# Kernel optimization log

Measured on AMD Instinct MI355X. Metric: run time of the kernel, lower is better.

Reference implementation:

```python
import jax, jax.numpy as jnp
import numpy as np

B, N, DIM = 2, 2048, 1024
HEADS, DIM_HEAD = 16, 64
ALIBI_HEADS = 8
NUM_MEM_KV = 4
SCALE = DIM_HEAD ** -0.5


def alibi_slopes(n):
    # standard ALiBi geometric slopes for power-of-2 head counts
    start = 2.0 ** (-8.0 / n)
    return jnp.array([start ** (k + 1) for k in range(n)], dtype=jnp.float32)


def alibi_bias(i, j, heads, total_heads):
    # symmetric ALiBi: bias = -|k_pos - q_pos| * slope; unbiased heads padded with zeros at front
    range_q = jnp.arange(j - i, j)          # query absolute positions (offset by mem kv)
    range_k = jnp.arange(j)
    rel = -jnp.abs(range_k[None, :] - range_q[:, None]).astype(jnp.float32)  # [i, j]
    slopes = alibi_slopes(heads)
    bias = slopes[:, None, None] * rel[None]                                  # [heads, i, j]
    pad = jnp.zeros((total_heads - heads, i, j), dtype=bias.dtype)
    return jnp.concatenate([pad, bias], axis=0)                               # [total_heads, i, j]


def setup_inputs() -> dict:
    key = jax.random.key(0)
    ks = jax.random.split(key, 7)
    w = lambda k, s: jax.random.normal(k, s, jnp.float32) * 0.02
    return {
        "x": jax.random.normal(ks[0], (B, N, DIM), jnp.float32),
        "mask": jnp.ones((B, N), dtype=bool),
        "Wq": w(ks[1], (DIM, HEADS * DIM_HEAD)),
        "Wk": w(ks[2], (DIM, HEADS * DIM_HEAD)),
        "Wv": w(ks[3], (DIM, HEADS * DIM_HEAD)),
        "Wo": w(ks[4], (HEADS * DIM_HEAD, DIM)),
        "mem_k": jax.random.normal(ks[5], (HEADS, NUM_MEM_KV, DIM_HEAD), jnp.float32),
        "mem_v": jax.random.normal(ks[6], (HEADS, NUM_MEM_KV, DIM_HEAD), jnp.float32),
    }


def reference(x, mask, Wq, Wk, Wv, Wo, mem_k, mem_v):
    b, n, _ = x.shape
    h, d, m = HEADS, DIM_HEAD, NUM_MEM_KV
    # QKV projections (Linear, no bias)
    q = (x @ Wq).reshape(b, n, h, d).transpose(0, 2, 1, 3)  # [b,h,n,d]
    k = (x @ Wk).reshape(b, n, h, d).transpose(0, 2, 1, 3)
    v = (x @ Wv).reshape(b, n, h, d).transpose(0, 2, 1, 3)
    # prepend learned memory key/values
    k = jnp.concatenate([jnp.broadcast_to(mem_k[None], (b, h, m, d)), k], axis=2)
    v = jnp.concatenate([jnp.broadcast_to(mem_v[None], (b, h, m, d)), v], axis=2)
    i, j = n, n + m
    # input mask padded with True over memory positions
    input_mask = jnp.concatenate([jnp.ones((b, m), dtype=bool), mask], axis=1)  # [b,j]
    # causal mask: key kj attendable by query qi iff kj - (j - i) <= qi (mem keys always visible)
    qpos = jnp.arange(i)[:, None]
    kpos = jnp.arange(j)[None, :]
    causal_allow = (kpos - (j - i)) <= qpos                                      # [i,j]
    allow = input_mask[:, None, None, :] & causal_allow[None, None]              # [b,1,i,j]
    bias = alibi_bias(i, j, ALIBI_HEADS, h)                                      # [h,i,j]
    scores = jnp.einsum('bhid,bhjd->bhij', q, k) * SCALE + bias[None]
    scores = jnp.where(allow, scores, jnp.finfo(scores.dtype).min)
    attn = jax.nn.softmax(scores, axis=-1)
    out = jnp.einsum('bhij,bhjd->bhid', attn, v)
    out = out.transpose(0, 2, 1, 3).reshape(b, n, h * d) @ Wo
    return out * mask[..., None].astype(out.dtype)
```

## Files before the change

kernel.cpp:

```cpp
#include <hip/hip_runtime.h>

typedef __bf16 bf16x8 __attribute__((ext_vector_type(8)));
typedef float f32x4 __attribute__((ext_vector_type(4)));
typedef unsigned short us8 __attribute__((ext_vector_type(8)));
typedef unsigned short ushort_t;
typedef unsigned int uint_t;

constexpr int BATCH = 2;
constexpr int SEQ   = 2048;
constexpr int DIM   = 1024;
constexpr int HEADS = 16;
constexpr int DH    = 64;
constexpr int NKV   = 4;
constexpr int KROWS = 2080;
constexpr int KVSTR = 133120;
constexpr float QSCALE = 0.18033688011112042f;

__device__ inline ushort_t f2bf(float f) {
  uint_t u = __builtin_bit_cast(uint_t, f);
  u += 0x7FFFu + ((u >> 16) & 1u);
  return (ushort_t)(u >> 16);
}

__device__ inline uint_t cvtpk(float a, float b) {
  uint_t r;
  asm("v_cvt_pk_bf16_f32 %0, %1, %2" : "=v"(r) : "v"(a), "v"(b));
  return r;
}

__device__ inline float ex2(float x) { return __builtin_amdgcn_exp2f(x); }

__device__ inline bf16x8 mk8(uint_t a, uint_t b, uint_t c, uint_t d) {
  union { uint_t u[4]; bf16x8 v; } x;
  x.u[0] = a; x.u[1] = b; x.u[2] = c; x.u[3] = d;
  return x.v;
}

__device__ inline size_t swz(int row, int k) {
  return ((size_t)(row >> 7) << 17) +
         (size_t)(((k >> 3) << 7) + (row & 127)) * 8 + (k & 7);
}

__device__ inline int koff(int j, int d) {
  return ((j >> 4) << 10) + ((d >> 3) << 7) + ((j & 15) << 3) + (d & 7);
}
__device__ inline int voff(int j, int d) {
  int w = j & 31;
  int kap = ((w & 12) << 1) | (w & 3) | ((w >> 4) << 2);
  return ((j >> 5) << 11) + ((kap >> 3) << 9) + (d << 3) + (kap & 7);
}

__device__ inline void g2l16(const ushort_t* g, ushort_t* l) {
  __builtin_amdgcn_global_load_lds(
      (const __attribute__((address_space(1))) void*)g,
      (__attribute__((address_space(3))) void*)l, 16, 0, 0);
}

__global__ __launch_bounds__(256) void prep_kernel(
    const float* __restrict__ x,
    const float* __restrict__ W0, const float* __restrict__ W1,
    const float* __restrict__ W2, const float* __restrict__ W3,
    const float* __restrict__ memk, const float* __restrict__ memv,
    ushort_t* __restrict__ xb,
    ushort_t* __restrict__ T0, ushort_t* __restrict__ T1,
    ushort_t* __restrict__ T2, ushort_t* __restrict__ T3,
    ushort_t* __restrict__ Vt, ushort_t* __restrict__ Ka)
{
  __shared__ float tile[32][33];
  int bid = blockIdx.x, t = threadIdx.x;
  if (bid < 2048) {
    int idx = bid * 256 + t;
    const float4* s = (const float4*)x;
    float4 a = s[idx * 2], bq = s[idx * 2 + 1];
    us8 o;
    o[0] = f2bf(a.x);  o[1] = f2bf(a.y);  o[2] = f2bf(a.z);  o[3] = f2bf(a.w);
    o[4] = f2bf(bq.x); o[5] = f2bf(bq.y); o[6] = f2bf(bq.z); o[7] = f2bf(bq.w);
    int e = idx * 8, row = e >> 10, k = e & 1023;
    *(us8*)&xb[swz(row, k)] = o;
  } else if (bid < 6144) {
    int tb = bid - 2048, z = tb >> 10, r2 = tb & 1023;
    int bx = r2 & 31, by = r2 >> 5;
    const float* W = (z == 0) ? W0 : (z == 1) ? W1 : (z == 2) ? W2 : W3;
    ushort_t* T = (z == 0) ? T0 : (z == 1) ? T1 : (z == 2) ? T2 : T3;
    float sc = (z == 0) ? QSCALE : 1.0f;
    int tx = t & 31, ty = t >> 5;
    int kb = bx * 32, nb = by * 32;
    for (int y = ty; y < 32; y += 8)
      tile[y][tx] = W[(size_t)(kb + y) * 1024 + nb + tx];
    __syncthreads();
    for (int y = ty; y < 32; y += 8)
      T[swz(nb + y, kb + tx)] = f2bf(tile[tx][y] * sc);
  } else {
    int idx = (bid - 6144) * 256 + t;
    if (idx < 8192) {
      int j = idx & 3, d = (idx >> 2) & 63, h = (idx >> 8) & 15, b = idx >> 12;
      Vt[(size_t)(b * 16 + h) * KVSTR + voff(j, d)] =
          f2bf(memv[((size_t)h * NKV + j) * DH + d]);
    } else if (idx < 16384) {
      int k2 = idx - 8192;
      int d = k2 & 63, j = (k2 >> 6) & 3, h = (k2 >> 8) & 15, b = k2 >> 12;
      Ka[(size_t)(b * 16 + h) * KVSTR + koff(j, d)] =
          f2bf(memk[((size_t)h * NKV + j) * DH + d]);
    }
  }
}

__global__ __launch_bounds__(256, 6) void gemm_bt(
    const ushort_t* __restrict__ A,
    const ushort_t* __restrict__ Wt0, const ushort_t* __restrict__ Wt1,
    const ushort_t* __restrict__ Wt2,
    ushort_t* __restrict__ C0, ushort_t* __restrict__ Ka,
    ushort_t* __restrict__ Vt)
{
  __shared__ ushort_t As[8192];
  __shared__ ushort_t Bs[4096];
  int bid = blockIdx.x;
  int xcd = bid & 7, g = bid >> 3;
  int z = g >> 6, rem = g & 63;
  int my = (xcd >> 1) * 8 + (rem >> 3);
  int nx = (xcd & 1) * 8 + (rem & 7);
  const ushort_t* Wt = (z == 1) ? Wt1 : (z == 2) ? Wt2 : Wt0;
  int t = threadIdx.x;
  int lane = t & 63, wave = t >> 6;
  int col = lane & 15, quad = lane >> 4;
  int m0 = my * 128, n0 = nx * 64;
  int moff = wave * 32;
  int nhalf = nx & 1;

  const ushort_t* Abase = A  + ((size_t)(m0 >> 7) << 17);
  const ushort_t* Bbase = Wt + ((size_t)(nx >> 1) << 17);
  int so = wave * 2048 + lane * 8;

  f32x4 acc[2][4] = {};

  for (int k0 = 0; k0 < DIM; k0 += 64) {
    __syncthreads();
    const ushort_t* Ak = Abase + ((size_t)k0 << 7);
    const ushort_t* Bk = Bbase + ((size_t)k0 << 7);
#pragma unroll
    for (int c2 = 0; c2 < 4; c2++)
      g2l16(Ak + so + c2 * 512, &As[so + c2 * 512]);
#pragma unroll
    for (int c2 = 0; c2 < 2; c2++) {
      int ko = wave * 2 + c2;
      g2l16(Bk + ko * 1024 + nhalf * 512 + lane * 8, &Bs[ko * 512 + lane * 8]);
    }
    __syncthreads();
#pragma unroll
    for (int kc = 0; kc < 2; kc++) {
      bf16x8 af[2], bfr[4];
#pragma unroll
      for (int mi = 0; mi < 2; mi++)
        af[mi] = *(const bf16x8*)&As[(kc * 4 + quad) * 1024 + (moff + mi * 16 + col) * 8];
#pragma unroll
      for (int ni = 0; ni < 4; ni++)
        bfr[ni] = *(const bf16x8*)&Bs[(kc * 4 + quad) * 512 + (ni * 16 + col) * 8];
#pragma unroll
      for (int mi = 0; mi < 2; mi++)
#pragma unroll
        for (int ni = 0; ni < 4; ni++)
          acc[mi][ni] = __builtin_amdgcn_mfma_f32_16x16x32_bf16(
              af[mi], bfr[ni], acc[mi][ni], 0, 0, 0);
    }
  }

  if (z == 0) {
#pragma unroll
    for (int mi = 0; mi < 2; mi++) {
      int row0 = m0 + moff + mi * 16 + quad * 4;
#pragma unroll
      for (int ni = 0; ni < 4; ni++) {
        int cn = n0 + ni * 16 + col;
#pragma unroll
        for (int r = 0; r < 4; r++)
          C0[swz(row0 + r, cn)] = f2bf(acc[mi][ni][r]);
      }
    }
  } else if (z == 1) {
#pragma unroll
    for (int mi = 0; mi < 2; mi++) {
      int gi = m0 + moff + mi * 16 + quad * 4;
      int bq = gi >> 11, i = gi & 2047;
#pragma unroll
      for (int ni = 0; ni < 4; ni++) {
        int feat = n0 + ni * 16 + col;
        int hh = feat >> 6, dd = feat & 63;
        size_t base = (size_t)(bq * 16 + hh) * KVSTR;
#pragma unroll
        for (int r = 0; r < 4; r++)
          Ka[base + koff(i + r + NKV, dd)] = f2bf(acc[mi][ni][r]);
      }
    }
  } else {
#pragma unroll
    for (int mi = 0; mi < 2; mi++) {
      int gi = m0 + moff + mi * 16 + quad * 4;
      int bq = gi >> 11, i = gi & 2047;
#pragma unroll
      for (int ni = 0; ni < 4; ni++) {
        int feat = n0 + ni * 16 + col;
        int hh = feat >> 6, dd = feat & 63;
        size_t vb = (size_t)(bq * 16 + hh) * KVSTR;
#pragma unroll
        for (int r = 0; r < 4; r++)
          Vt[vb + voff(i + r + NKV, dd)] = f2bf(acc[mi][ni][r]);
      }
    }
  }
}

__global__ __launch_bounds__(256, 4) void gemm_out64(
    const ushort_t* __restrict__ A, const ushort_t* __restrict__ Wt,
    float* __restrict__ Cf)
{
  __shared__ ushort_t As[4096];
  __shared__ ushort_t Bs[4096];
  int bid = blockIdx.x;
  int xcd = bid & 7, g = bid >> 3;
  int my = xcd * 8 + (g >> 4);
  int nx = g & 15;
  int t = threadIdx.x;
  int lane = t & 63, wave = t >> 6;
  int col = lane & 15, quad = lane >> 4;
  int m0 = my * 64, n0 = nx * 64;
  int mhalf = my & 1;
  int nhalf = nx & 1;

  const ushort_t* Abase = A  + ((size_t)(my >> 1) << 17);
  const ushort_t* Bbase = Wt + ((size_t)(nx >> 1) << 17);

  f32x4 acc[4] = {};

  for (int k0 = 0; k0 < DIM; k0 += 64) {
    __syncthreads();
    const ushort_t* Ak = Abase + ((size_t)k0 << 7);
    const ushort_t* Bk = Bbase + ((size_t)k0 << 7);
#pragma unroll
    for (int c2 = 0; c2 < 2; c2++) {
      int ko = wave * 2 + c2;
      g2l16(Ak + ko * 1024 + mhalf * 512 + lane * 8, &As[ko * 512 + lane * 8]);
      g2l16(Bk + ko * 1024 + nhalf * 512 + lane * 8, &Bs[ko * 512 + lane * 8]);
    }
    __syncthreads();
#pragma unroll
    for (int kc = 0; kc < 2; kc++) {
      bf16x8 af, bfr[4];
      af = *(const bf16x8*)&As[(kc * 4 + quad) * 512 + (wave * 16 + col) * 8];
#pragma unroll
      for (int ni = 0; ni < 4; ni++)
        bfr[ni] = *(const bf16x8*)&Bs[(kc * 4 + quad) * 512 + (ni * 16 + col) * 8];
#pragma unroll
      for (int ni = 0; ni < 4; ni++)
        acc[ni] = __builtin_amdgcn_mfma_f32_16x16x32_bf16(
            af, bfr[ni], acc[ni], 0, 0, 0);
    }
  }

  int row0 = m0 + wave * 16 + quad * 4;
#pragma unroll
  for (int ni = 0; ni < 4; ni++) {
    int cn = n0 + ni * 16 + col;
#pragma unroll
    for (int r = 0; r < 4; r++)
      Cf[(size_t)(row0 + r) * DIM + cn] = acc[ni][r];
  }
}

#define SUBITER(jbX, jpref, K0, K1, K2, K3, V0, V1, V2, V3)                   \
  {                                                                           \
    f32x4 s0a = {}, s1a = {}, s0b = {}, s1b = {};                             \
    __builtin_amdgcn_s_setprio(1);                                            \
    s0a = __builtin_amdgcn_mfma_f32_16x16x32_bf16(K0, qa0, s0a, 0, 0, 0);     \
    s0a = __builtin_amdgcn_mfma_f32_16x16x32_bf16(K1, qa1, s0a, 0, 0, 0);     \
    s1a = __builtin_amdgcn_mfma_f32_16x16x32_bf16(K2, qa0, s1a, 0, 0, 0);     \
    s1a = __builtin_amdgcn_mfma_f32_16x16x32_bf16(K3, qa1, s1a, 0, 0, 0);     \
    s0b = __builtin_amdgcn_mfma_f32_16x16x32_bf16(K0, qb0, s0b, 0, 0, 0);     \
    s0b = __builtin_amdgcn_mfma_f32_16x16x32_bf16(K1, qb1, s0b, 0, 0, 0);     \
    s1b = __builtin_amdgcn_mfma_f32_16x16x32_bf16(K2, qb0, s1b, 0, 0, 0);     \
    s1b = __builtin_amdgcn_mfma_f32_16x16x32_bf16(K3, qb1, s1b, 0, 0, 0);     \
    __builtin_amdgcn_s_setprio(0);                                            \
    int jc = (jpref) > 2048 ? 2048 : (jpref);                                 \
    int aK = jc * 64 + kOff;                                                  \
    K0 = *(const bf16x8*)&Kbh[aK];                                            \
    K1 = *(const bf16x8*)&Kbh[aK + 512];                                      \
    K2 = *(const bf16x8*)&Kbh[aK + 1024];                                     \
    K3 = *(const bf16x8*)&Kbh[aK + 1536];                                     \
    float fD0 = (float)((jbX) + quad * 4 - i0 - col - NKV);                   \
    bf16x8 pa, pb;                                                            \
    {                                                                         \
      f32x4 e0, e1;                                                           \
      if ((jbX) <= i0 - 27) {                                                 \
        _Pragma("unroll")                                                     \
        for (int r = 0; r < 4; r++) {                                         \
          e0[r] = ex2(fmaf(slope2, fD0 + (float)r, s0a[r]));                  \
          e1[r] = ex2(fmaf(slope2, fD0 + 16.0f + (float)r, s1a[r]));          \
        }                                                                     \
      } else {                                                                \
        _Pragma("unroll")                                                     \
        for (int r = 0; r < 4; r++) {                                         \
          float f0 = fD0 + (float)r, f1 = fD0 + 16.0f + (float)r;             \
          float w0 = fmaf(slope2, f0, s0a[r]);                                \
          float w1 = fmaf(slope2, f1, s1a[r]);                                \
          w0 = (f0 <= 0.0f) ? w0 : -1e30f;                                    \
          w1 = (f1 <= 0.0f) ? w1 : -1e30f;                                    \
          e0[r] = ex2(w0); e1[r] = ex2(w1);                                   \
        }                                                                     \
      }                                                                       \
      pa = mk8(cvtpk(e0[0], e0[1]), cvtpk(e0[2], e0[3]),                      \
               cvtpk(e1[0], e1[1]), cvtpk(e1[2], e1[3]));                     \
    }                                                                         \
    {                                                                         \
      float fDb = fD0 - 16.0f;                                                \
      f32x4 e0, e1;                                                           \
      if ((jbX) <= i0 - 11) {                                                 \
        _Pragma("unroll")                                                     \
        for (int r = 0; r < 4; r++) {                                         \
          e0[r] = ex2(fmaf(slope2, fDb + (float)r, s0b[r]));                  \
          e1[r] = ex2(fmaf(slope2, fDb + 16.0f + (float)r, s1b[r]));          \
        }                                                                     \
      } else {                                                                \
        _Pragma("unroll")                                                     \
        for (int r = 0; r < 4; r++) {                                         \
          float f0 = fDb + (float)r, f1 = fDb + 16.0f + (float)r;             \
          float w0 = fmaf(slope2, f0, s0b[r]);                                \
          float w1 = fmaf(slope2, f1, s1b[r]);                                \
          w0 = (f0 <= 0.0f) ? w0 : -1e30f;                                    \
          w1 = (f1 <= 0.0f) ? w1 : -1e30f;                                    \
          e0[r] = ex2(w0); e1[r] = ex2(w1);                                   \
        }                                                                     \
      }                                                                       \
      pb = mk8(cvtpk(e0[0], e0[1]), cvtpk(e0[2], e0[3]),                      \
               cvtpk(e1[0], e1[1]), cvtpk(e1[2], e1[3]));                     \
    }                                                                         \
    __builtin_amdgcn_s_setprio(1);                                            \
    o0a = __builtin_amdgcn_mfma_f32_16x16x32_bf16(pa, V0, o0a, 0, 0, 0);      \
    o1a = __builtin_amdgcn_mfma_f32_16x16x32_bf16(pa, V1, o1a, 0, 0, 0);      \
    o2a = __builtin_amdgcn_mfma_f32_16x16x32_bf16(pa, V2, o2a, 0, 0, 0);      \
    o3a = __builtin_amdgcn_mfma_f32_16x16x32_bf16(pa, V3, o3a, 0, 0, 0);      \
    ola = __builtin_amdgcn_mfma_f32_16x16x32_bf16(pa, ones, ola, 0, 0, 0);    \
    o0b = __builtin_amdgcn_mfma_f32_16x16x32_bf16(pb, V0, o0b, 0, 0, 0);      \
    o1b = __builtin_amdgcn_mfma_f32_16x16x32_bf16(pb, V1, o1b, 0, 0, 0);      \
    o2b = __builtin_amdgcn_mfma_f32_16x16x32_bf16(pb, V2, o2b, 0, 0, 0);      \
    o3b = __builtin_amdgcn_mfma_f32_16x16x32_bf16(pb, V3, o3b, 0, 0, 0);      \
    olb = __builtin_amdgcn_mfma_f32_16x16x32_bf16(pb, ones, olb, 0, 0, 0);    \
    __builtin_amdgcn_s_setprio(0);                                            \
    int aV = jc * 64 + vOff;                                                  \
    V0 = *(const bf16x8*)&Vbh[aV];                                            \
    V1 = *(const bf16x8*)&Vbh[aV + 128];                                      \
    V2 = *(const bf16x8*)&Vbh[aV + 256];                                      \
    V3 = *(const bf16x8*)&Vbh[aV + 384];                                      \
  }

__global__ __launch_bounds__(256) void attn_kernel(
    const ushort_t* __restrict__ Q, const ushort_t* __restrict__ Ka,
    const ushort_t* __restrict__ Vt, ushort_t* __restrict__ AO)
{
  __shared__ __align__(16) float Cmb[2][10][64][4];
  int t = threadIdx.x, lane = t & 63, wave = t >> 6;
  int col = lane & 15, quad = lane >> 4;
  int bid = blockIdx.x;
  int xcd = bid & 7, slot = bid >> 3;
  int bh = xcd + 8 * (slot >> 4);
  int b = bh >> 4, h = bh & 15;
  int u = slot & 15;
  int pi = u * 2 + (wave >> 1);
  int h2 = wave & 1;
  int p2 = wave >> 1;
  float slope2 = (h < 8) ? 0.0f : exp2f(-(float)(h - 7)) * 1.4426950408889634f;

  const ushort_t* Kbh = Ka + (size_t)bh * KVSTR;
  const ushort_t* Vbh = Vt + (size_t)bh * KVSTR;

  us8 ones_u = {0x3F80, 0x3F80, 0x3F80, 0x3F80, 0x3F80, 0x3F80, 0x3F80, 0x3F80};
  bf16x8 ones = __builtin_bit_cast(bf16x8, ones_u);

  int kOff = quad * 128 + col * 8;
  int vOff = quad * 512 + col * 8;

  for (int hv = 0; hv < 2; hv++) {
    int s = hv ? 63 - pi : pi;
    int i0 = s * 32;
    int jend = ((i0 + 67) >> 5) << 5;

    bf16x8 qa0 = *(const bf16x8*)&Q[swz(b * SEQ + i0 + col, h * DH + quad * 8)];
    bf16x8 qa1 = *(const bf16x8*)&Q[swz(b * SEQ + i0 + col, h * DH + 32 + quad * 8)];
    bf16x8 qb0 = *(const bf16x8*)&Q[swz(b * SEQ + i0 + 16 + col, h * DH + quad * 8)];
    bf16x8 qb1 = *(const bf16x8*)&Q[swz(b * SEQ + i0 + 16 + col, h * DH + 32 + quad * 8)];

    f32x4 o0a = {}, o1a = {}, o2a = {}, o3a = {}, ola = {};
    f32x4 o0b = {}, o1b = {}, o2b = {}, o3b = {}, olb = {};

    bf16x8 ka0, ka1, ka2, ka3, va0, va1, va2, va3;
    bf16x8 kb0, kb1, kb2, kb3, vb0, vb1, vb2, vb3;
    int jb0 = h2 * 32;
    {
      int aK = jb0 * 64 + kOff, aV = jb0 * 64 + vOff;
      ka0 = *(const bf16x8*)&Kbh[aK];
      ka1 = *(const bf16x8*)&Kbh[aK + 512];
      ka2 = *(const bf16x8*)&Kbh[aK + 1024];
      ka3 = *(const bf16x8*)&Kbh[aK + 1536];
      va0 = *(const bf16x8*)&Vbh[aV];
      va1 = *(const bf16x8*)&Vbh[aV + 128];
      va2 = *(const bf16x8*)&Vbh[aV + 256];
      va3 = *(const bf16x8*)&Vbh[aV + 384];
      int j1 = jb0 + 64; if (j1 > 2048) j1 = 2048;
      int bK = j1 * 64 + kOff, bV = j1 * 64 + vOff;
      kb0 = *(const bf16x8*)&Kbh[bK];
      kb1 = *(const bf16x8*)&Kbh[bK + 512];
      kb2 = *(const bf16x8*)&Kbh[bK + 1024];
      kb3 = *(const bf16x8*)&Kbh[bK + 1536];
      vb0 = *(const bf16x8*)&Vbh[bV];
      vb1 = *(const bf16x8*)&Vbh[bV + 128];
      vb2 = *(const bf16x8*)&Vbh[bV + 256];
      vb3 = *(const bf16x8*)&Vbh[bV + 384];
    }

    int ntrip = (jend - jb0 + 127) >> 7;
    int jb = jb0;
#pragma unroll 1
    for (int tr = 0; tr < ntrip; tr++, jb += 128) {
      SUBITER(jb, jb + 128, ka0, ka1, ka2, ka3, va0, va1, va2, va3);
      SUBITER(jb + 64, jb + 192, kb0, kb1, kb2, kb3, vb0, vb1, vb2, vb3);
    }

    if (h2 == 1) {
      *(f32x4*)&Cmb[p2][0][lane][0] = o0a;
      *(f32x4*)&Cmb[p2][1][lane][0] = o1a;
      *(f32x4*)&Cmb[p2][2][lane][0] = o2a;
      *(f32x4*)&Cmb[p2][3][lane][0] = o3a;
      *(f32x4*)&Cmb[p2][4][lane][0] = ola;
      *(f32x4*)&Cmb[p2][5][lane][0] = o0b;
      *(f32x4*)&Cmb[p2][6][lane][0] = o1b;
      *(f32x4*)&Cmb[p2][7][lane][0] = o2b;
      *(f32x4*)&Cmb[p2][8][lane][0] = o3b;
      *(f32x4*)&Cmb[p2][9][lane][0] = olb;
    }
    __syncthreads();
    if (h2 == 0) {
      o0a += *(const f32x4*)&Cmb[p2][0][lane][0];
      o1a += *(const f32x4*)&Cmb[p2][1][lane][0];
      o2a += *(const f32x4*)&Cmb[p2][2][lane][0];
      o3a += *(const f32x4*)&Cmb[p2][3][lane][0];
      ola += *(const f32x4*)&Cmb[p2][4][lane][0];
      o0b += *(const f32x4*)&Cmb[p2][5][lane][0];
      o1b += *(const f32x4*)&Cmb[p2][6][lane][0];
      o2b += *(const f32x4*)&Cmb[p2][7][lane][0];
      o3b += *(const f32x4*)&Cmb[p2][8][lane][0];
      olb += *(const f32x4*)&Cmb[p2][9][lane][0];
#pragma unroll
      for (int r = 0; r < 4; r++) {
        float linv = __builtin_amdgcn_rcpf(ola[r]);
        int row = b * SEQ + i0 + quad * 4 + r;
        AO[swz(row, h * DH + col)]      = f2bf(o0a[r] * linv);
        AO[swz(row, h * DH + 16 + col)] = f2bf(o1a[r] * linv);
        AO[swz(row, h * DH + 32 + col)] = f2bf(o2a[r] * linv);
        AO[swz(row, h * DH + 48 + col)] = f2bf(o3a[r] * linv);
      }
#pragma unroll
      for (int r = 0; r < 4; r++) {
        float linv = __builtin_amdgcn_rcpf(olb[r]);
        int row = b * SEQ + i0 + 16 + quad * 4 + r;
        AO[swz(row, h * DH + col)]      = f2bf(o0b[r] * linv);
        AO[swz(row, h * DH + 16 + col)] = f2bf(o1b[r] * linv);
        AO[swz(row, h * DH + 32 + col)] = f2bf(o2b[r] * linv);
        AO[swz(row, h * DH + 48 + col)] = f2bf(o3b[r] * linv);
      }
    }
    __syncthreads();
  }
}
#undef SUBITER

extern "C" void kernel_launch(void* const* d_in, const int* in_sizes, int n_in,
                              void* d_out, int out_size, void* d_ws, size_t ws_size,
                              hipStream_t stream)
{
  const float* x    = (const float*)d_in[0];
  const float* Wq   = (const float*)d_in[2];
  const float* Wk   = (const float*)d_in[3];
  const float* Wv   = (const float*)d_in[4];
  const float* Wo   = (const float*)d_in[5];
  const float* memk = (const float*)d_in[6];
  const float* memv = (const float*)d_in[7];
  float* out = (float*)d_out;

  char* ws = (char*)d_ws;
  size_t off = 0;
  auto alloc = [&](size_t bytes) {
    char* p = ws + off;
    off += (bytes + 255) & ~(size_t)255;
    return p;
  };
  ushort_t* WqT = (ushort_t*)alloc((size_t)1024 * 1024 * 2);
  ushort_t* WkT = (ushort_t*)alloc((size_t)1024 * 1024 * 2);
  ushort_t* WvT = (ushort_t*)alloc((size_t)1024 * 1024 * 2);
  ushort_t* WoT = (ushort_t*)alloc((size_t)1024 * 1024 * 2);
  ushort_t* xb  = (ushort_t*)alloc((size_t)4096 * 1024 * 2);
  ushort_t* Qb  = (ushort_t*)alloc((size_t)4096 * 1024 * 2);
  ushort_t* Ka  = (ushort_t*)alloc((size_t)32 * KVSTR * 2);
  ushort_t* Vt  = (ushort_t*)alloc((size_t)32 * KVSTR * 2);
  ushort_t* AO  = xb;

  prep_kernel<<<dim3(6208), dim3(256), 0, stream>>>(
      x, Wq, Wk, Wv, Wo, memk, memv, xb, WqT, WkT, WvT, WoT, Vt, Ka);
  gemm_bt<<<dim3(1536), dim3(256), 0, stream>>>(xb, WqT, WkT, WvT, Qb, Ka, Vt);
  attn_kernel<<<dim3(512), dim3(256), 0, stream>>>(Qb, Ka, Vt, AO);
  gemm_out64<<<dim3(1024), dim3(256), 0, stream>>>(AO, WoT, out);
}
```

Baseline: 175.5 us.

## Process paired causal query strips together sharing each K/V register load

Instead of looping over the two balanced query strips (pi and 63-pi) one after another, each wave now keeps both strips' Q fragments and accumulators live and, for every key block, runs the score/softmax/PV sequence for the long strip and, while still within its causal range, for the short strip. Each K/V fragment loaded from global memory is thereby reused by two query strips, roughly halving K/V load traffic and dropping one pass of loop prologue. The cost is doubled accumulator and Q register pressure, which may reduce occupancy or cause spills, and a branch inside the inner loop.

```diff
diff --git a/kernel.cpp b/kernel.cpp
--- a/kernel.cpp
+++ b/kernel.cpp
@@ -266,30 +266,26 @@
   }
 }
 
-#define SUBITER(jbX, jpref, K0, K1, K2, K3, V0, V1, V2, V3)                   \
+#define STRIPC(jbX, I0, Q00, Q01, Q10, Q11,                                   \
+               O0A, O1A, O2A, O3A, OLA, O0B, O1B, O2B, O3B, OLB,              \
+               K0, K1, K2, K3, V0, V1, V2, V3)                                \
   {                                                                           \
     f32x4 s0a = {}, s1a = {}, s0b = {}, s1b = {};                             \
     __builtin_amdgcn_s_setprio(1);                                            \
-    s0a = __builtin_amdgcn_mfma_f32_16x16x32_bf16(K0, qa0, s0a, 0, 0, 0);     \
-    s0a = __builtin_amdgcn_mfma_f32_16x16x32_bf16(K1, qa1, s0a, 0, 0, 0);     \
-    s1a = __builtin_amdgcn_mfma_f32_16x16x32_bf16(K2, qa0, s1a, 0, 0, 0);     \
-    s1a = __builtin_amdgcn_mfma_f32_16x16x32_bf16(K3, qa1, s1a, 0, 0, 0);     \
-    s0b = __builtin_amdgcn_mfma_f32_16x16x32_bf16(K0, qb0, s0b, 0, 0, 0);     \
-    s0b = __builtin_amdgcn_mfma_f32_16x16x32_bf16(K1, qb1, s0b, 0, 0, 0);     \
-    s1b = __builtin_amdgcn_mfma_f32_16x16x32_bf16(K2, qb0, s1b, 0, 0, 0);     \
-    s1b = __builtin_amdgcn_mfma_f32_16x16x32_bf16(K3, qb1, s1b, 0, 0, 0);     \
+    s0a = __builtin_amdgcn_mfma_f32_16x16x32_bf16(K0, Q00, s0a, 0, 0, 0);     \
+    s0a = __builtin_amdgcn_mfma_f32_16x16x32_bf16(K1, Q01, s0a, 0, 0, 0);     \
+    s1a = __builtin_amdgcn_mfma_f32_16x16x32_bf16(K2, Q00, s1a, 0, 0, 0);     \
+    s1a = __builtin_amdgcn_mfma_f32_16x16x32_bf16(K3, Q01, s1a, 0, 0, 0);     \
+    s0b = __builtin_amdgcn_mfma_f32_16x16x32_bf16(K0, Q10, s0b, 0, 0, 0);     \
+    s0b = __builtin_amdgcn_mfma_f32_16x16x32_bf16(K1, Q11, s0b, 0, 0, 0);     \
+    s1b = __builtin_amdgcn_mfma_f32_16x16x32_bf16(K2, Q10, s1b, 0, 0, 0);     \
+    s1b = __builtin_amdgcn_mfma_f32_16x16x32_bf16(K3, Q11, s1b, 0, 0, 0);     \
     __builtin_amdgcn_s_setprio(0);                                            \
-    int jc = (jpref) > 2048 ? 2048 : (jpref);                                 \
-    int aK = jc * 64 + kOff;                                                  \
-    K0 = *(const bf16x8*)&Kbh[aK];                                            \
-    K1 = *(const bf16x8*)&Kbh[aK + 512];                                      \
-    K2 = *(const bf16x8*)&Kbh[aK + 1024];                                     \
-    K3 = *(const bf16x8*)&Kbh[aK + 1536];                                     \
-    float fD0 = (float)((jbX) + quad * 4 - i0 - col - NKV);                   \
+    float fD0 = (float)((jbX) + quad * 4 - (I0) - col - NKV);                 \
     bf16x8 pa, pb;                                                            \
     {                                                                         \
       f32x4 e0, e1;                                                           \
-      if ((jbX) <= i0 - 27) {                                                 \
+      if ((jbX) <= (I0) - 27) {                                               \
         _Pragma("unroll")                                                     \
         for (int r = 0; r < 4; r++) {                                         \
           e0[r] = ex2(fmaf(slope2, fD0 + (float)r, s0a[r]));                  \
@@ -312,7 +308,7 @@
     {                                                                         \
       float fDb = fD0 - 16.0f;                                                \
       f32x4 e0, e1;                                                           \
-      if ((jbX) <= i0 - 11) {                                                 \
+      if ((jbX) <= (I0) - 11) {                                               \
         _Pragma("unroll")                                                     \
         for (int r = 0; r < 4; r++) {                                         \
           e0[r] = ex2(fmaf(slope2, fDb + (float)r, s0b[r]));                  \
@@ -333,17 +329,35 @@
                cvtpk(e1[0], e1[1]), cvtpk(e1[2], e1[3]));                     \
     }                                                                         \
     __builtin_amdgcn_s_setprio(1);                                            \
-    o0a = __builtin_amdgcn_mfma_f32_16x16x32_bf16(pa, V0, o0a, 0, 0, 0);      \
-    o1a = __builtin_amdgcn_mfma_f32_16x16x32_bf16(pa, V1, o1a, 0, 0, 0);      \
-    o2a = __builtin_amdgcn_mfma_f32_16x16x32_bf16(pa, V2, o2a, 0, 0, 0);      \
-    o3a = __builtin_amdgcn_mfma_f32_16x16x32_bf16(pa, V3, o3a, 0, 0, 0);      \
-    ola = __builtin_amdgcn_mfma_f32_16x16x32_bf16(pa, ones, ola, 0, 0, 0);    \
-    o0b = __builtin_amdgcn_mfma_f32_16x16x32_bf16(pb, V0, o0b, 0, 0, 0);      \
-    o1b = __builtin_amdgcn_mfma_f32_16x16x32_bf16(pb, V1, o1b, 0, 0, 0);      \
-    o2b = __builtin_amdgcn_mfma_f32_16x16x32_bf16(pb, V2, o2b, 0, 0, 0);      \
-    o3b = __builtin_amdgcn_mfma_f32_16x16x32_bf16(pb, V3, o3b, 0, 0, 0);      \
-    olb = __builtin_amdgcn_mfma_f32_16x16x32_bf16(pb, ones, olb, 0, 0, 0);    \
+    O0A = __builtin_amdgcn_mfma_f32_16x16x32_bf16(pa, V0, O0A, 0, 0, 0);      \
+    O1A = __builtin_amdgcn_mfma_f32_16x16x32_bf16(pa, V1, O1A, 0, 0, 0);      \
+    O2A = __builtin_amdgcn_mfma_f32_16x16x32_bf16(pa, V2, O2A, 0, 0, 0);      \
+    O3A = __builtin_amdgcn_mfma_f32_16x16x32_bf16(pa, V3, O3A, 0, 0, 0);      \
+    OLA = __builtin_amdgcn_mfma_f32_16x16x32_bf16(pa, ones, OLA, 0, 0, 0);    \
+    O0B = __builtin_amdgcn_mfma_f32_16x16x32_bf16(pb, V0, O0B, 0, 0, 0);      \
+    O1B = __builtin_amdgcn_mfma_f32_16x16x32_bf16(pb, V1, O1B, 0, 0, 0);      \
+    O2B = __builtin_amdgcn_mfma_f32_16x16x32_bf16(pb, V2, O2B, 0, 0, 0);      \
+    O3B = __builtin_amdgcn_mfma_f32_16x16x32_bf16(pb, V3, O3B, 0, 0, 0);      \
+    OLB = __builtin_amdgcn_mfma_f32_16x16x32_bf16(pb, ones, OLB, 0, 0, 0);    \
     __builtin_amdgcn_s_setprio(0);                                            \
+  }
+
+#define SUBITER(jbX, jpref, K0, K1, K2, K3, V0, V1, V2, V3)                   \
+  {                                                                           \
+    STRIPC(jbX, i0y, qy00, qy01, qy10, qy11,                                  \
+           yo0a, yo1a, yo2a, yo3a, yla, yo0b, yo1b, yo2b, yo3b, ylb,          \
+           K0, K1, K2, K3, V0, V1, V2, V3);                                   \
+    if ((jbX) < jendx) {                                                      \
+      STRIPC(jbX, i0x, qx00, qx01, qx10, qx11,                                \
+             xo0a, xo1a, xo2a, xo3a, xla, xo0b, xo1b, xo2b, xo3b, xlb,        \
+             K0, K1, K2, K3, V0, V1, V2, V3);                                 \
+    }                                                                         \
+    int jc = (jpref) > 2048 ? 2048 : (jpref);                                 \
+    int aK = jc * 64 + kOff;                                                  \
+    K0 = *(const bf16x8*)&Kbh[aK];                                            \
+    K1 = *(const bf16x8*)&Kbh[aK + 512];                                      \
+    K2 = *(const bf16x8*)&Kbh[aK + 1024];                                     \
+    K3 = *(const bf16x8*)&Kbh[aK + 1536];                                     \
     int aV = jc * 64 + vOff;                                                  \
     V0 = *(const bf16x8*)&Vbh[aV];                                            \
     V1 = *(const bf16x8*)&Vbh[aV + 128];                                      \
@@ -377,99 +391,149 @@
   int kOff = quad * 128 + col * 8;
   int vOff = quad * 512 + col * 8;
 
-  for (int hv = 0; hv < 2; hv++) {
-    int s = hv ? 63 - pi : pi;
-    int i0 = s * 32;
-    int jend = ((i0 + 67) >> 5) << 5;
-
-    bf16x8 qa0 = *(const bf16x8*)&Q[swz(b * SEQ + i0 + col, h * DH + quad * 8)];
-    bf16x8 qa1 = *(const bf16x8*)&Q[swz(b * SEQ + i0 + col, h * DH + 32 + quad * 8)];
-    bf16x8 qb0 = *(const bf16x8*)&Q[swz(b * SEQ + i0 + 16 + col, h * DH + quad * 8)];
-    bf16x8 qb1 = *(const bf16x8*)&Q[swz(b * SEQ + i0 + 16 + col, h * DH + 32 + quad * 8)];
-
-    f32x4 o0a = {}, o1a = {}, o2a = {}, o3a = {}, ola = {};
-    f32x4 o0b = {}, o1b = {}, o2b = {}, o3b = {}, olb = {};
-
-    bf16x8 ka0, ka1, ka2, ka3, va0, va1, va2, va3;
-    bf16x8 kb0, kb1, kb2, kb3, vb0, vb1, vb2, vb3;
-    int jb0 = h2 * 32;
-    {
-      int aK = jb0 * 64 + kOff, aV = jb0 * 64 + vOff;
-      ka0 = *(const bf16x8*)&Kbh[aK];
-      ka1 = *(const bf16x8*)&Kbh[aK + 512];
-      ka2 = *(const bf16x8*)&Kbh[aK + 1024];
-      ka3 = *(const bf16x8*)&Kbh[aK + 1536];
-      va0 = *(const bf16x8*)&Vbh[aV];
-      va1 = *(const bf16x8*)&Vbh[aV + 128];
-      va2 = *(const bf16x8*)&Vbh[aV + 256];
-      va3 = *(const bf16x8*)&Vbh[aV + 384];
-      int j1 = jb0 + 64; if (j1 > 2048) j1 = 2048;
-      int bK = j1 * 64 + kOff, bV = j1 * 64 + vOff;
-      kb0 = *(const bf16x8*)&Kbh[bK];
-      kb1 = *(const bf16x8*)&Kbh[bK + 512];
-      kb2 = *(const bf16x8*)&Kbh[bK + 1024];
-      kb3 = *(const bf16x8*)&Kbh[bK + 1536];
-      vb0 = *(const bf16x8*)&Vbh[bV];
-      vb1 = *(const bf16x8*)&Vbh[bV + 128];
-      vb2 = *(const bf16x8*)&Vbh[bV + 256];
-      vb3 = *(const bf16x8*)&Vbh[bV + 384];
-    }
-
-    int ntrip = (jend - jb0 + 127) >> 7;
-    int jb = jb0;
+  int i0x = pi * 32;
+  int i0y = 2016 - pi * 32;
+  int jendx = ((i0x + 67) >> 5) << 5;
+  int jendy = ((i0y + 67) >> 5) << 5;
+
+  bf16x8 qx00 = *(const bf16x8*)&Q[swz(b * SEQ + i0x + col, h * DH + quad * 8)];
+  bf16x8 qx01 = *(const bf16x8*)&Q[swz(b * SEQ + i0x + col, h * DH + 32 + quad * 8)];
+  bf16x8 qx10 = *(const bf16x8*)&Q[swz(b * SEQ + i0x + 16 + col, h * DH + quad * 8)];
+  bf16x8 qx11 = *(const bf16x8*)&Q[swz(b * SEQ + i0x + 16 + col, h * DH + 32 + quad * 8)];
+  bf16x8 qy00 = *(const bf16x8*)&Q[swz(b * SEQ + i0y + col, h * DH + quad * 8)];
+  bf16x8 qy01 = *(const bf16x8*)&Q[swz(b * SEQ + i0y + col, h * DH + 32 + quad * 8)];
+  bf16x8 qy10 = *(const bf16x8*)&Q[swz(b * SEQ + i0y + 16 + col, h * DH + quad * 8)];
+  bf16x8 qy11 = *(const bf16x8*)&Q[swz(b * SEQ + i0y + 16 + col, h * DH + 32 + quad * 8)];
+
+  f32x4 xo0a = {}, xo1a = {}, xo2a = {}, xo3a = {}, xla = {};
+  f32x4 xo0b = {}, xo1b = {}, xo2b = {}, xo3b = {}, xlb = {};
+  f32x4 yo0a = {}, yo1a = {}, yo2a = {}, yo3a = {}, yla = {};
+  f32x4 yo0b = {}, yo1b = {}, yo2b = {}, yo3b = {}, ylb = {};
+
+  bf16x8 ka0, ka1, ka2, ka3, va0, va1, va2, va3;
+  bf16x8 kb0, kb1, kb2, kb3, vb0, vb1, vb2, vb3;
+  int jb0 = h2 * 32;
+  {
+    int aK = jb0 * 64 + kOff, aV = jb0 * 64 + vOff;
+    ka0 = *(const bf16x8*)&Kbh[aK];
+    ka1 = *(const bf16x8*)&Kbh[aK + 512];
+    ka2 = *(const bf16x8*)&Kbh[aK + 1024];
+    ka3 = *(const bf16x8*)&Kbh[aK + 1536];
+    va0 = *(const bf16x8*)&Vbh[aV];
+    va1 = *(const bf16x8*)&Vbh[aV + 128];
+    va2 = *(const bf16x8*)&Vbh[aV + 256];
+    va3 = *(const bf16x8*)&Vbh[aV + 384];
+    int j1 = jb0 + 64;
+    int bK = j1 * 64 + kOff, bV = j1 * 64 + vOff;
+    kb0 = *(const bf16x8*)&Kbh[bK];
+    kb1 = *(const bf16x8*)&Kbh[bK + 512];
+    kb2 = *(const bf16x8*)&Kbh[bK + 1024];
+    kb3 = *(const bf16x8*)&Kbh[bK + 1536];
+    vb0 = *(const bf16x8*)&Vbh[bV];
+    vb1 = *(const bf16x8*)&Vbh[bV + 128];
+    vb2 = *(const bf16x8*)&Vbh[bV + 256];
+    vb3 = *(const bf16x8*)&Vbh[bV + 384];
+  }
+
+  int ntrip = (jendy - jb0 + 127) >> 7;
+  int jb = jb0;
 #pragma unroll 1
-    for (int tr = 0; tr < ntrip; tr++, jb += 128) {
-      SUBITER(jb, jb + 128, ka0, ka1, ka2, ka3, va0, va1, va2, va3);
-      SUBITER(jb + 64, jb + 192, kb0, kb1, kb2, kb3, vb0, vb1, vb2, vb3);
-    }
-
-    if (h2 == 1) {
-      *(f32x4*)&Cmb[p2][0][lane][0] = o0a;
-      *(f32x4*)&Cmb[p2][1][lane][0] = o1a;
-      *(f32x4*)&Cmb[p2][2][lane][0] = o2a;
-      *(f32x4*)&Cmb[p2][3][lane][0] = o3a;
-      *(f32x4*)&Cmb[p2][4][lane][0] = ola;
-      *(f32x4*)&Cmb[p2][5][lane][0] = o0b;
-      *(f32x4*)&Cmb[p2][6][lane][0] = o1b;
-      *(f32x4*)&Cmb[p2][7][lane][0] = o2b;
-      *(f32x4*)&Cmb[p2][8][lane][0] = o3b;
-      *(f32x4*)&Cmb[p2][9][lane][0] = olb;
-    }
-    __syncthreads();
-    if (h2 == 0) {
-      o0a += *(const f32x4*)&Cmb[p2][0][lane][0];
-      o1a += *(const f32x4*)&Cmb[p2][1][lane][0];
-      o2a += *(const f32x4*)&Cmb[p2][2][lane][0];
-      o3a += *(const f32x4*)&Cmb[p2][3][lane][0];
-      ola += *(const f32x4*)&Cmb[p2][4][lane][0];
-      o0b += *(const f32x4*)&Cmb[p2][5][lane][0];
-      o1b += *(const f32x4*)&Cmb[p2][6][lane][0];
-      o2b += *(const f32x4*)&Cmb[p2][7][lane][0];
-      o3b += *(const f32x4*)&Cmb[p2][8][lane][0];
-      olb += *(const f32x4*)&Cmb[p2][9][lane][0];
-#pragma unroll
-      for (int r = 0; r < 4; r++) {
-        float linv = __builtin_amdgcn_rcpf(ola[r]);
-        int row = b * SEQ + i0 + quad * 4 + r;
-        AO[swz(row, h * DH + col)]      = f2bf(o0a[r] * linv);
-        AO[swz(row, h * DH + 16 + col)] = f2bf(o1a[r] * linv);
-        AO[swz(row, h * DH + 32 + col)] = f2bf(o2a[r] * linv);
-        AO[swz(row, h * DH + 48 + col)] = f2bf(o3a[r] * linv);
-      }
-#pragma unroll
-      for (int r = 0; r < 4; r++) {
-        float linv = __builtin_amdgcn_rcpf(olb[r]);
-        int row = b * SEQ + i0 + 16 + quad * 4 + r;
-        AO[swz(row, h * DH + col)]      = f2bf(o0b[r] * linv);
-        AO[swz(row, h * DH + 16 + col)] = f2bf(o1b[r] * linv);
-        AO[swz(row, h * DH + 32 + col)] = f2bf(o2b[r] * linv);
-        AO[swz(row, h * DH + 48 + col)] = f2bf(o3b[r] * linv);
-      }
-    }
-    __syncthreads();
+  for (int tr = 0; tr < ntrip; tr++, jb += 128) {
+    SUBITER(jb, jb + 128, ka0, ka1, ka2, ka3, va0, va1, va2, va3);
+    SUBITER(jb + 64, jb + 192, kb0, kb1, kb2, kb3, vb0, vb1, vb2, vb3);
+  }
+
+  if (h2 == 1) {
+    *(f32x4*)&Cmb[p2][0][lane][0] = yo0a;
+    *(f32x4*)&Cmb[p2][1][lane][0] = yo1a;
+    *(f32x4*)&Cmb[p2][2][lane][0] = yo2a;
+    *(f32x4*)&Cmb[p2][3][lane][0] = yo3a;
+    *(f32x4*)&Cmb[p2][4][lane][0] = yla;
+    *(f32x4*)&Cmb[p2][5][lane][0] = yo0b;
+    *(f32x4*)&Cmb[p2][6][lane][0] = yo1b;
+    *(f32x4*)&Cmb[p2][7][lane][0] = yo2b;
+    *(f32x4*)&Cmb[p2][8][lane][0] = yo3b;
+    *(f32x4*)&Cmb[p2][9][lane][0] = ylb;
+  }
+  __syncthreads();
+  if (h2 == 0) {
+    yo0a += *(const f32x4*)&Cmb[p2][0][lane][0];
+    yo1a += *(const f32x4*)&Cmb[p2][1][lane][0];
+    yo2a += *(const f32x4*)&Cmb[p2][2][lane][0];
+    yo3a += *(const f32x4*)&Cmb[p2][3][lane][0];
+    yla  += *(const f32x4*)&Cmb[p2][4][lane][0];
+    yo0b += *(const f32x4*)&Cmb[p2][5][lane][0];
+    yo1b += *(const f32x4*)&Cmb[p2][6][lane][0];
+    yo2b += *(const f32x4*)&Cmb[p2][7][lane][0];
+    yo3b += *(const f32x4*)&Cmb[p2][8][lane][0];
+    ylb  += *(const f32x4*)&Cmb[p2][9][lane][0];
+#pragma unroll
+    for (int r = 0; r < 4; r++) {
+      float linv = __builtin_amdgcn_rcpf(yla[r]);
+      int row = b * SEQ + i0y + quad * 4 + r;
+      AO[swz(row, h * DH + col)]      = f2bf(yo0a[r] * linv);
+      AO[swz(row, h * DH + 16 + col)] = f2bf(yo1a[r] * linv);
+      AO[swz(row, h * DH + 32 + col)] = f2bf(yo2a[r] * linv);
+      AO[swz(row, h * DH + 48 + col)] = f2bf(yo3a[r] * linv);
+    }
+#pragma unroll
+    for (int r = 0; r < 4; r++) {
+      float linv = __builtin_amdgcn_rcpf(ylb[r]);
+      int row = b * SEQ + i0y + 16 + quad * 4 + r;
+      AO[swz(row, h * DH + col)]      = f2bf(yo0b[r] * linv);
+      AO[swz(row, h * DH + 16 + col)] = f2bf(yo1b[r] * linv);
+      AO[swz(row, h * DH + 32 + col)] = f2bf(yo2b[r] * linv);
+      AO[swz(row, h * DH + 48 + col)] = f2bf(yo3b[r] * linv);
+    }
+  }
+  __syncthreads();
+
+  if (h2 == 1) {
+    *(f32x4*)&Cmb[p2][0][lane][0] = xo0a;
+    *(f32x4*)&Cmb[p2][1][lane][0] = xo1a;
+    *(f32x4*)&Cmb[p2][2][lane][0] = xo2a;
+    *(f32x4*)&Cmb[p2][3][lane][0] = xo3a;
+    *(f32x4*)&Cmb[p2][4][lane][0] = xla;
+    *(f32x4*)&Cmb[p2][5][lane][0] = xo0b;
+    *(f32x4*)&Cmb[p2][6][lane][0] = xo1b;
+    *(f32x4*)&Cmb[p2][7][lane][0] = xo2b;
+    *(f32x4*)&Cmb[p2][8][lane][0] = xo3b;
+    *(f32x4*)&Cmb[p2][9][lane][0] = xlb;
+  }
+  __syncthreads();
+  if (h2 == 0) {
+    xo0a += *(const f32x4*)&Cmb[p2][0][lane][0];
+    xo1a += *(const f32x4*)&Cmb[p2][1][lane][0];
+    xo2a += *(const f32x4*)&Cmb[p2][2][lane][0];
+    xo3a += *(const f32x4*)&Cmb[p2][3][lane][0];
+    xla  += *(const f32x4*)&Cmb[p2][4][lane][0];
+    xo0b += *(const f32x4*)&Cmb[p2][5][lane][0];
+    xo1b += *(const f32x4*)&Cmb[p2][6][lane][0];
+    xo2b += *(const f32x4*)&Cmb[p2][7][lane][0];
+    xo3b += *(const f32x4*)&Cmb[p2][8][lane][0];
+    xlb  += *(const f32x4*)&Cmb[p2][9][lane][0];
+#pragma unroll
+    for (int r = 0; r < 4; r++) {
+      float linv = __builtin_amdgcn_rcpf(xla[r]);
+      int row = b * SEQ + i0x + quad * 4 + r;
+      AO[swz(row, h * DH + col)]      = f2bf(xo0a[r] * linv);
+      AO[swz(row, h * DH + 16 + col)] = f2bf(xo1a[r] * linv);
+      AO[swz(row, h * DH + 32 + col)] = f2bf(xo2a[r] * linv);
+      AO[swz(row, h * DH + 48 + col)] = f2bf(xo3a[r] * linv);
+    }
+#pragma unroll
+    for (int r = 0; r < 4; r++) {
+      float linv = __builtin_amdgcn_rcpf(xlb[r]);
+      int row = b * SEQ + i0x + 16 + quad * 4 + r;
+      AO[swz(row, h * DH + col)]      = f2bf(xo0b[r] * linv);
+      AO[swz(row, h * DH + 16 + col)] = f2bf(xo1b[r] * linv);
+      AO[swz(row, h * DH + 32 + col)] = f2bf(xo2b[r] * linv);
+      AO[swz(row, h * DH + 48 + col)] = f2bf(xo3b[r] * linv);
+    }
   }
 }
 #undef SUBITER
+#undef STRIPC
 
 extern "C" void kernel_launch(void* const* d_in, const int* in_sizes, int n_in,
                               void* d_out, int out_size, void* d_ws, size_t ws_size,
```

Result: slower. 188.5 us (+7.4%).
